# Kernel tuning notes

Hardware: AMD Instinct MI355X
Metric: run time of the kernel (lower is better)

Reference implementation:

```python
import jax, jax.numpy as jnp
import numpy as np

GAMMA = 1.0
SENTINEL = 999.0

def spike_mp(in_mat, gamma):
    # in_mat: [B, N, F]. Weighted-median-style threshold crossing (TTFS spike time).
    in_mat = jnp.sort(in_mat, axis=1)
    B, N, F = in_mat.shape
    cs = jnp.cumsum(in_mat, axis=1) + gamma
    denom = jnp.arange(1, N + 1, dtype=in_mat.dtype)[None, :, None]
    cs = cs / denom  # candidate spike times
    pad_hi = jnp.full((B, 1, F), SENTINEL, dtype=in_mat.dtype)
    pad_lo = jnp.zeros((B, 1, F), dtype=in_mat.dtype)
    arr_1 = jnp.concatenate([pad_hi, cs], axis=1)      # [B, N+1, F]
    arr_2 = jnp.concatenate([in_mat, pad_lo], axis=1)  # [B, N+1, F]
    out = jnp.where(arr_1 > arr_2, SENTINEL, arr_1)
    out = jnp.min(out, axis=1)                          # [B, F]
    out = jnp.where(out == SENTINEL, arr_1[:, -1], out)
    return out

def reference(x, W):
    # x: [B, In], W: [In, Out]. The original python concat-loop is a tile ->
    # expressed here via broadcasting to avoid materializing copies early.
    xb = x[:, :, None]                      # [B, In, 1]
    plus_in = 2.0 + xb                      # 1 + x + 1
    minus_in = 2.0 - xb                     # 1 - x + 1
    plus_w = (0.5 * (3.0 + W))[None]        # [1, In, Out]
    minus_w = (0.5 * (3.0 - W))[None]
    z_plus = jnp.concatenate([plus_in + plus_w, minus_in + minus_w], axis=1)   # [B, 2In, Out]
    z_minus = jnp.concatenate([plus_in + minus_w, minus_in + plus_w], axis=1)  # [B, 2In, Out]
    return jax.nn.relu(spike_mp(z_plus, GAMMA) - spike_mp(z_minus, GAMMA))

def setup_inputs() -> dict:
    key = jax.random.key(0)
    k1, k2 = jax.random.split(key)
    x = jax.random.uniform(k1, (32, 1024), dtype=jnp.float32)
    # GlorotNormal-ish init, clipped to [-3, 3] per the constraint
    std = np.sqrt(2.0 / (1024 + 512)).astype(np.float32)
    W = jnp.clip(jax.random.normal(k2, (1024, 512), dtype=jnp.float32) * std, -3.0, 3.0)
    return {"x": x, "W": W}
```

## Files before the change

### kernel.cpp

```cpp
#include <hip/hip_runtime.h>
#include <math.h>

#define NB 32
#define NN 1024
#define NF 512

__global__ __launch_bounds__(256) void transpose_w_k(const float* __restrict__ W,
                                                     float* __restrict__ Wt) {
    __shared__ float tile[32][33];
    int n0 = blockIdx.x * 32;
    int f0 = blockIdx.y * 32;
    int tx = threadIdx.x & 31;
    int ty = threadIdx.x >> 5;
#pragma unroll
    for (int r = 0; r < 32; r += 8) {
        tile[ty + r][tx] = W[(n0 + ty + r) * NF + (f0 + tx)];
    }
    __syncthreads();
#pragma unroll
    for (int r = 0; r < 32; r += 8) {
        Wt[(f0 + ty + r) * NN + (n0 + tx)] = tile[tx][ty + r];
    }
}

#define DPP_XOR1        0xB1
#define DPP_XOR2        0x4E
#define DPP_HALF_MIRROR 0x141
#define DPP_MIRROR      0x140
#define DPP_BCAST15     0x142
#define DPP_BCAST31     0x143

template <int CTRL>
__device__ __forceinline__ float dpp_mov(float v) {
    return __int_as_float(__builtin_amdgcn_update_dpp(
        0, __float_as_int(v), CTRL, 0xf, 0xf, true));
}

__device__ __forceinline__ float wave_sum_u(float v) {
    v += dpp_mov<DPP_XOR1>(v);
    v += dpp_mov<DPP_XOR2>(v);
    v += dpp_mov<DPP_HALF_MIRROR>(v);
    v += dpp_mov<DPP_MIRROR>(v);
    v += dpp_mov<DPP_BCAST15>(v);
    v += dpp_mov<DPP_BCAST31>(v);
    return __int_as_float(__builtin_amdgcn_readlane(__float_as_int(v), 63));
}
__device__ __forceinline__ float wave_max_u(float v) {
    v = fmaxf(v, dpp_mov<DPP_XOR1>(v));
    v = fmaxf(v, dpp_mov<DPP_XOR2>(v));
    v = fmaxf(v, dpp_mov<DPP_HALF_MIRROR>(v));
    v = fmaxf(v, dpp_mov<DPP_MIRROR>(v));
    v = fmaxf(v, dpp_mov<DPP_BCAST15>(v));
    v = fmaxf(v, dpp_mov<DPP_BCAST31>(v));
    return __int_as_float(__builtin_amdgcn_readlane(__float_as_int(v), 63));
}

__device__ __forceinline__ float fast_sqrt(float v) { return __builtin_amdgcn_sqrtf(v); }
__device__ __forceinline__ float fast_rcp(float v)  { return __builtin_amdgcn_rcpf(v); }

#define COLD_SOLVE(MARR, SV, MV, NEGV, RESV)                                     \
    if (NEGV) {                                                                  \
        float t_ = fminf(fmaxf(2.0f * (SV - fast_sqrt(SV)) * (1.0f/1024.0f), 0.0f), MV); \
        _Pragma("unroll 1")                                                      \
        for (int s_ = 0; s_ < 20; ++s_) {                                        \
            float ss_ = 0.f; int c_ = 0;                                         \
            _Pragma("unroll")                                                    \
            for (int j_ = 0; j_ < 16; ++j_) {                                    \
                bool pr_ = (MARR[j_] >= t_);                                     \
                c_ += (int)__popcll(__ballot(pr_));                              \
                ss_ += pr_ ? MARR[j_] : 0.0f;                                    \
            }                                                                    \
            ss_ = wave_sum_u(ss_);                                               \
            float fc_ = (float)c_;                                               \
            float E_ = ss_ - t_ * fc_;                                           \
            float d_ = (E_ >= 1.0f) ? 2.0f * (E_ - fast_sqrt(E_)) : (E_ - 1.0f); \
            t_ = fminf(fmaxf(t_ + d_ * fast_rcp(fc_), 0.0f), MV);                \
        }                                                                        \
        RESV = -t_;                                                              \
    } else {                                                                     \
        float u_ = (1.0f - SV) * (1.0f/1024.0f);                                 \
        _Pragma("unroll 1")                                                      \
        for (int s_ = 0; s_ < 12; ++s_) {                                        \
            float s2_ = 0.f; int c2_ = 0;                                        \
            _Pragma("unroll")                                                    \
            for (int j_ = 0; j_ < 16; ++j_) {                                    \
                bool pr_ = (MARR[j_] <= u_);                                     \
                c2_ += (int)__popcll(__ballot(pr_));                             \
                s2_ += pr_ ? MARR[j_] : 0.0f;                                    \
            }                                                                    \
            s2_ = wave_sum_u(s2_);                                               \
            u_ = (1.0f - SV + s2_) * fast_rcp(1024.0f + (float)c2_);             \
        }                                                                        \
        RESV = u_;                                                               \
    }

__global__ __launch_bounds__(256) void spike_main_k(const float* __restrict__ x,
                                                    const float* __restrict__ W,
                                                    const float* __restrict__ Wt,
                                                    int use_wt,
                                                    float* __restrict__ out) {
    int bid  = blockIdx.x;
    int b    = bid >> 7;
    int fg   = bid & 127;
    int wave = threadIdx.x >> 6;
    int lane = threadIdx.x & 63;
    int f    = fg * 4 + wave;

    float mp[16], mm[16];
    float sp0 = 0.f, sm0 = 0.f, xp0 = 0.f, xm0 = 0.f;

    if (use_wt) {
        const float4* x4 = reinterpret_cast<const float4*>(x + (size_t)b * NN);
        const float4* w4 = reinterpret_cast<const float4*>(Wt + (size_t)f * NN);
#pragma unroll
        for (int j = 0; j < 4; ++j) {
            float4 xv = x4[lane + 64 * j];
            float4 wv = w4[lane + 64 * j];
            float ap, am;
            ap = fabsf(xv.x + 0.5f * wv.x); am = fabsf(xv.x - 0.5f * wv.x);
            mp[4*j+0] = ap; mm[4*j+0] = am; sp0 += ap; sm0 += am;
            xp0 = fmaxf(xp0, ap); xm0 = fmaxf(xm0, am);
            ap = fabsf(xv.y + 0.5f * wv.y); am = fabsf(xv.y - 0.5f * wv.y);
            mp[4*j+1] = ap; mm[4*j+1] = am; sp0 += ap; sm0 += am;
            xp0 = fmaxf(xp0, ap); xm0 = fmaxf(xm0, am);
            ap = fabsf(xv.z + 0.5f * wv.z); am = fabsf(xv.z - 0.5f * wv.z);
            mp[4*j+2] = ap; mm[4*j+2] = am; sp0 += ap; sm0 += am;
            xp0 = fmaxf(xp0, ap); xm0 = fmaxf(xm0, am);
            ap = fabsf(xv.w + 0.5f * wv.w); am = fabsf(xv.w - 0.5f * wv.w);
            mp[4*j+3] = ap; mm[4*j+3] = am; sp0 += ap; sm0 += am;
            xp0 = fmaxf(xp0, ap); xm0 = fmaxf(xm0, am);
        }
    } else {
#pragma unroll
        for (int j = 0; j < 16; ++j) {
            int n = lane + 64 * j;
            float xv = x[(size_t)b * NN + n];
            float wv = W[(size_t)n * NF + f];
            float ap = fabsf(xv + 0.5f * wv);
            float am = fabsf(xv - 0.5f * wv);
            mp[j] = ap; mm[j] = am;
            sp0 += ap; sm0 += am;
            xp0 = fmaxf(xp0, ap); xm0 = fmaxf(xm0, am);
        }
    }

#pragma unroll
    for (int j = 0; j < 16; ++j) {
        asm volatile("" : "+v"(mp[j]), "+v"(mm[j]));
    }

    float Sp = wave_sum_u(sp0);
    float Sm = wave_sum_u(sm0);
    float Mp = wave_max_u(xp0);
    float Mm = wave_max_u(xm0);

    const bool neg_p = (Sp >= 1.0f);
    const bool neg_m = (Sm >= 1.0f);

    float up_out, um_out;

    if (neg_p && neg_m) {
        float tp = fminf(fmaxf(2.0f * (Sp - fast_sqrt(Sp)) * (1.0f / 1024.0f), 0.0f), Mp);
        float tm = fminf(fmaxf(2.0f * (Sm - fast_sqrt(Sm)) * (1.0f / 1024.0f), 0.0f), Mm);
#pragma unroll
        for (int s = 0; s < 5; ++s) {
            float ssp = 0.f, ssm = 0.f;
            int cp = 0, cm = 0;
#pragma unroll
            for (int j = 0; j < 16; ++j) {
                bool prp = (mp[j] >= tp);
                bool prm = (mm[j] >= tm);
                cp += (int)__popcll(__ballot(prp));
                cm += (int)__popcll(__ballot(prm));
                ssp += prp ? mp[j] : 0.0f;
                ssm += prm ? mm[j] : 0.0f;
            }
            ssp = wave_sum_u(ssp);
            ssm = wave_sum_u(ssm);
            float fcp = (float)cp, fcm = (float)cm;
            float Ep = ssp - tp * fcp;
            float Em = ssm - tm * fcm;
            float dp = (Ep >= 1.0f) ? 2.0f * (Ep - fast_sqrt(Ep)) : (Ep - 1.0f);
            float dm = (Em >= 1.0f) ? 2.0f * (Em - fast_sqrt(Em)) : (Em - 1.0f);
            tp = fminf(fmaxf(tp + dp * fast_rcp(fcp), 0.0f), Mp);
            tm = fminf(fmaxf(tm + dm * fast_rcp(fcm), 0.0f), Mm);
        }
        up_out = -tp;
        um_out = -tm;
    } else {
        COLD_SOLVE(mp, Sp, Mp, neg_p, up_out);
        COLD_SOLVE(mm, Sm, Mm, neg_m, um_out);
    }

    if (lane == 0) out[(size_t)b * NF + f] = fmaxf(up_out - um_out, 0.0f);
}

extern "C" void kernel_launch(void* const* d_in, const int* in_sizes, int n_in,
                              void* d_out, int out_size, void* d_ws, size_t ws_size,
                              hipStream_t stream) {
    const float* x = (const float*)d_in[0];
    const float* W = (const float*)d_in[1];
    float* out = (float*)d_out;

    const size_t wt_bytes = (size_t)NN * NF * sizeof(float);
    int use_wt = (ws_size >= wt_bytes) ? 1 : 0;
    float* Wt = (float*)d_ws;

    if (use_wt) {
        dim3 g(NN / 32, NF / 32);
        transpose_w_k<<<g, 256, 0, stream>>>(W, Wt);
    }
    spike_main_k<<<NB * (NF / 4), 256, 0, stream>>>(x, W, Wt, use_wt, out);
}
```

Before: 31.07 us.

## Use secant-based threshold solve and process two features per wave

```diff
diff --git a/kernel.cpp b/kernel.cpp
--- a/kernel.cpp
+++ b/kernel.cpp
@@ -57,6 +57,55 @@
 
 __device__ __forceinline__ float fast_sqrt(float v) { return __builtin_amdgcn_sqrtf(v); }
 __device__ __forceinline__ float fast_rcp(float v)  { return __builtin_amdgcn_rcpf(v); }
+
+#define FAST_SOLVE(MP, MM, SP, SM, MPX, MMX, TP_OUT, TM_OUT)                          \
+    {                                                                                 \
+        float tpp_ = 0.0f, Epp_ = SP;                                                 \
+        float tmp2_ = 0.0f, Emp_ = SM;                                                \
+        float tp_ = fminf(2.0f * (SP - fast_sqrt(SP)) * (1.0f/1024.0f), MPX);         \
+        float tm_ = fminf(2.0f * (SM - fast_sqrt(SM)) * (1.0f/1024.0f), MMX);         \
+        _Pragma("unroll")                                                             \
+        for (int s_ = 0; s_ < 5; ++s_) {                                              \
+            float ep_ = 0.f, em_ = 0.f;                                               \
+            _Pragma("unroll")                                                         \
+            for (int j_ = 0; j_ < 16; ++j_) {                                         \
+                ep_ += fmaxf(MP[j_] - tp_, 0.0f);                                     \
+                em_ += fmaxf(MM[j_] - tm_, 0.0f);                                     \
+            }                                                                         \
+            ep_ = wave_sum_u(ep_);                                                    \
+            em_ = wave_sum_u(em_);                                                    \
+            float rp_, rm_, rpp_, rmp_;                                               \
+            if (s_ < 3) { rp_ = fast_sqrt(ep_);  rm_ = fast_sqrt(em_);                \
+                          rpp_ = fast_sqrt(Epp_); rmp_ = fast_sqrt(Emp_); }           \
+            else        { rp_ = ep_; rm_ = em_; rpp_ = Epp_; rmp_ = Emp_; }           \
+            float denp_ = rp_ - rpp_, denm_ = rm_ - rmp_;                             \
+            float stp_ = (denp_ != 0.0f)                                              \
+                       ? (tp_ - tpp_) * (1.0f - rp_) * fast_rcp(denp_) : 0.0f;        \
+            float stm_ = (denm_ != 0.0f)                                              \
+                       ? (tm_ - tmp2_) * (1.0f - rm_) * fast_rcp(denm_) : 0.0f;       \
+            tpp_ = tp_; Epp_ = ep_; tmp2_ = tm_; Emp_ = em_;                          \
+            tp_ = fminf(fmaxf(tp_ + stp_, 0.0f), MPX);                                \
+            tm_ = fminf(fmaxf(tm_ + stm_, 0.0f), MMX);                                \
+        }                                                                             \
+        _Pragma("unroll")                                                             \
+        for (int q_ = 0; q_ < 2; ++q_) {                                              \
+            float ep_ = 0.f, cp_ = 0.f, em_ = 0.f, cm_ = 0.f;                         \
+            _Pragma("unroll")                                                         \
+            for (int j_ = 0; j_ < 16; ++j_) {                                         \
+                float dp_ = MP[j_] - tp_;                                             \
+                float dm_ = MM[j_] - tm_;                                             \
+                bool ap_ = (dp_ >= 0.0f);                                             \
+                bool am_ = (dm_ >= 0.0f);                                             \
+                ep_ += ap_ ? dp_ : 0.0f;  cp_ += ap_ ? 1.0f : 0.0f;                   \
+                em_ += am_ ? dm_ : 0.0f;  cm_ += am_ ? 1.0f : 0.0f;                   \
+            }                                                                         \
+            ep_ = wave_sum_u(ep_); cp_ = wave_sum_u(cp_);                             \
+            em_ = wave_sum_u(em_); cm_ = wave_sum_u(cm_);                             \
+            tp_ = fminf(fmaxf(tp_ + (ep_ - 1.0f) * fast_rcp(cp_), 0.0f), MPX);        \
+            tm_ = fminf(fmaxf(tm_ + (em_ - 1.0f) * fast_rcp(cm_), 0.0f), MMX);        \
+        }                                                                             \
+        TP_OUT = tp_; TM_OUT = tm_;                                                   \
+    }
 
 #define COLD_SOLVE(MARR, SV, MV, NEGV, RESV)                                     \
     if (NEGV) {                                                                  \
@@ -94,105 +143,96 @@
         RESV = u_;                                                               \
     }
 
+#define SETUP4(XV, WV, MP, MM, BASE, SPV, SMV, XPV, XMV)                         \
+    {                                                                            \
+        float ap_, am_;                                                          \
+        ap_ = fabsf(XV.x + 0.5f * WV.x); am_ = fabsf(XV.x - 0.5f * WV.x);        \
+        MP[BASE+0] = ap_; MM[BASE+0] = am_; SPV += ap_; SMV += am_;              \
+        XPV = fmaxf(XPV, ap_); XMV = fmaxf(XMV, am_);                            \
+        ap_ = fabsf(XV.y + 0.5f * WV.y); am_ = fabsf(XV.y - 0.5f * WV.y);        \
+        MP[BASE+1] = ap_; MM[BASE+1] = am_; SPV += ap_; SMV += am_;              \
+        XPV = fmaxf(XPV, ap_); XMV = fmaxf(XMV, am_);                            \
+        ap_ = fabsf(XV.z + 0.5f * WV.z); am_ = fabsf(XV.z - 0.5f * WV.z);        \
+        MP[BASE+2] = ap_; MM[BASE+2] = am_; SPV += ap_; SMV += am_;              \
+        XPV = fmaxf(XPV, ap_); XMV = fmaxf(XMV, am_);                            \
+        ap_ = fabsf(XV.w + 0.5f * WV.w); am_ = fabsf(XV.w - 0.5f * WV.w);        \
+        MP[BASE+3] = ap_; MM[BASE+3] = am_; SPV += ap_; SMV += am_;              \
+        XPV = fmaxf(XPV, ap_); XMV = fmaxf(XMV, am_);                            \
+    }
+
 __global__ __launch_bounds__(256) void spike_main_k(const float* __restrict__ x,
-                                                    const float* __restrict__ W,
                                                     const float* __restrict__ Wt,
-                                                    int use_wt,
                                                     float* __restrict__ out) {
     int bid  = blockIdx.x;
-    int b    = bid >> 7;
-    int fg   = bid & 127;
+    int b    = bid >> 6;
+    int fg   = bid & 63;
     int wave = threadIdx.x >> 6;
     int lane = threadIdx.x & 63;
-    int f    = fg * 4 + wave;
-
-    float mp[16], mm[16];
-    float sp0 = 0.f, sm0 = 0.f, xp0 = 0.f, xm0 = 0.f;
-
-    if (use_wt) {
-        const float4* x4 = reinterpret_cast<const float4*>(x + (size_t)b * NN);
-        const float4* w4 = reinterpret_cast<const float4*>(Wt + (size_t)f * NN);
-#pragma unroll
-        for (int j = 0; j < 4; ++j) {
-            float4 xv = x4[lane + 64 * j];
-            float4 wv = w4[lane + 64 * j];
-            float ap, am;
-            ap = fabsf(xv.x + 0.5f * wv.x); am = fabsf(xv.x - 0.5f * wv.x);
-            mp[4*j+0] = ap; mm[4*j+0] = am; sp0 += ap; sm0 += am;
-            xp0 = fmaxf(xp0, ap); xm0 = fmaxf(xm0, am);
-            ap = fabsf(xv.y + 0.5f * wv.y); am = fabsf(xv.y - 0.5f * wv.y);
-            mp[4*j+1] = ap; mm[4*j+1] = am; sp0 += ap; sm0 += am;
-            xp0 = fmaxf(xp0, ap); xm0 = fmaxf(xm0, am);
-            ap = fabsf(xv.z + 0.5f * wv.z); am = fabsf(xv.z - 0.5f * wv.z);
-            mp[4*j+2] = ap; mm[4*j+2] = am; sp0 += ap; sm0 += am;
-            xp0 = fmaxf(xp0, ap); xm0 = fmaxf(xm0, am);
-            ap = fabsf(xv.w + 0.5f * wv.w); am = fabsf(xv.w - 0.5f * wv.w);
-            mp[4*j+3] = ap; mm[4*j+3] = am; sp0 += ap; sm0 += am;
-            xp0 = fmaxf(xp0, ap); xm0 = fmaxf(xm0, am);
-        }
-    } else {
-#pragma unroll
-        for (int j = 0; j < 16; ++j) {
-            int n = lane + 64 * j;
-            float xv = x[(size_t)b * NN + n];
-            float wv = W[(size_t)n * NF + f];
-            float ap = fabsf(xv + 0.5f * wv);
-            float am = fabsf(xv - 0.5f * wv);
-            mp[j] = ap; mm[j] = am;
-            sp0 += ap; sm0 += am;
-            xp0 = fmaxf(xp0, ap); xm0 = fmaxf(xm0, am);
-        }
-    }
+    int f1   = fg * 4 + wave;
+    int f2   = f1 + 256;
+
+    const float4* x4  = reinterpret_cast<const float4*>(x + (size_t)b * NN);
+    const float4* wa4 = reinterpret_cast<const float4*>(Wt + (size_t)f1 * NN);
+    const float4* wb4 = reinterpret_cast<const float4*>(Wt + (size_t)f2 * NN);
+
+    float4 xr0 = x4[lane +   0], xr1 = x4[lane +  64],
+           xr2 = x4[lane + 128], xr3 = x4[lane + 192];
+    float4 wa0 = wa4[lane +   0], wa1 = wa4[lane +  64],
+           wa2 = wa4[lane + 128], wa3 = wa4[lane + 192];
+    float4 wb0 = wb4[lane +   0], wb1 = wb4[lane +  64],
+           wb2 = wb4[lane + 128], wb3 = wb4[lane + 192];
+
+    float mp1[16], mm1[16], mp2[16], mm2[16];
+    float sp1 = 0.f, sm1 = 0.f, xp1 = 0.f, xm1 = 0.f;
+    float sp2 = 0.f, sm2 = 0.f, xp2 = 0.f, xm2 = 0.f;
+
+    SETUP4(xr0, wa0, mp1, mm1,  0, sp1, sm1, xp1, xm1);
+    SETUP4(xr1, wa1, mp1, mm1,  4, sp1, sm1, xp1, xm1);
+    SETUP4(xr2, wa2, mp1, mm1,  8, sp1, sm1, xp1, xm1);
+    SETUP4(xr3, wa3, mp1, mm1, 12, sp1, sm1, xp1, xm1);
+    SETUP4(xr0, wb0, mp2, mm2,  0, sp2, sm2, xp2, xm2);
+    SETUP4(xr1, wb1, mp2, mm2,  4, sp2, sm2, xp2, xm2);
+    SETUP4(xr2, wb2, mp2, mm2,  8, sp2, sm2, xp2, xm2);
+    SETUP4(xr3, wb3, mp2, mm2, 12, sp2, sm2, xp2, xm2);
 
 #pragma unroll
     for (int j = 0; j < 16; ++j) {
-        asm volatile("" : "+v"(mp[j]), "+v"(mm[j]));
-    }
-
-    float Sp = wave_sum_u(sp0);
-    float Sm = wave_sum_u(sm0);
-    float Mp = wave_max_u(xp0);
-    float Mm = wave_max_u(xm0);
-
-    const bool neg_p = (Sp >= 1.0f);
-    const bool neg_m = (Sm >= 1.0f);
-
-    float up_out, um_out;
-
-    if (neg_p && neg_m) {
-        float tp = fminf(fmaxf(2.0f * (Sp - fast_sqrt(Sp)) * (1.0f / 1024.0f), 0.0f), Mp);
-        float tm = fminf(fmaxf(2.0f * (Sm - fast_sqrt(Sm)) * (1.0f / 1024.0f), 0.0f), Mm);
-#pragma unroll
-        for (int s = 0; s < 5; ++s) {
-            float ssp = 0.f, ssm = 0.f;
-            int cp = 0, cm = 0;
-#pragma unroll
-            for (int j = 0; j < 16; ++j) {
-                bool prp = (mp[j] >= tp);
-                bool prm = (mm[j] >= tm);
-                cp += (int)__popcll(__ballot(prp));
-                cm += (int)__popcll(__ballot(prm));
-                ssp += prp ? mp[j] : 0.0f;
-                ssm += prm ? mm[j] : 0.0f;
-            }
-            ssp = wave_sum_u(ssp);
-            ssm = wave_sum_u(ssm);
-            float fcp = (float)cp, fcm = (float)cm;
-            float Ep = ssp - tp * fcp;
-            float Em = ssm - tm * fcm;
-            float dp = (Ep >= 1.0f) ? 2.0f * (Ep - fast_sqrt(Ep)) : (Ep - 1.0f);
-            float dm = (Em >= 1.0f) ? 2.0f * (Em - fast_sqrt(Em)) : (Em - 1.0f);
-            tp = fminf(fmaxf(tp + dp * fast_rcp(fcp), 0.0f), Mp);
-            tm = fminf(fmaxf(tm + dm * fast_rcp(fcm), 0.0f), Mm);
-        }
-        up_out = -tp;
-        um_out = -tm;
+        asm volatile("" : "+v"(mp1[j]), "+v"(mm1[j]), "+v"(mp2[j]), "+v"(mm2[j]));
+    }
+
+    float Sp1 = wave_sum_u(sp1), Sm1 = wave_sum_u(sm1);
+    float Mp1 = wave_max_u(xp1), Mm1 = wave_max_u(xm1);
+    float Sp2 = wave_sum_u(sp2), Sm2 = wave_sum_u(sm2);
+    float Mp2 = wave_max_u(xp2), Mm2 = wave_max_u(xm2);
+
+    float o1, o2;
+
+    if (Sp1 >= 1.0f && Sm1 >= 1.0f) {
+        float tp1, tm1;
+        FAST_SOLVE(mp1, mm1, Sp1, Sm1, Mp1, Mm1, tp1, tm1);
+        o1 = fmaxf(tm1 - tp1, 0.0f);
     } else {
-        COLD_SOLVE(mp, Sp, Mp, neg_p, up_out);
-        COLD_SOLVE(mm, Sm, Mm, neg_m, um_out);
-    }
-
-    if (lane == 0) out[(size_t)b * NF + f] = fmaxf(up_out - um_out, 0.0f);
+        float up1, um1;
+        COLD_SOLVE(mp1, Sp1, Mp1, (Sp1 >= 1.0f), up1);
+        COLD_SOLVE(mm1, Sm1, Mm1, (Sm1 >= 1.0f), um1);
+        o1 = fmaxf(up1 - um1, 0.0f);
+    }
+
+    if (Sp2 >= 1.0f && Sm2 >= 1.0f) {
+        float tp2, tm2;
+        FAST_SOLVE(mp2, mm2, Sp2, Sm2, Mp2, Mm2, tp2, tm2);
+        o2 = fmaxf(tm2 - tp2, 0.0f);
+    } else {
+        float up2, um2;
+        COLD_SOLVE(mp2, Sp2, Mp2, (Sp2 >= 1.0f), up2);
+        COLD_SOLVE(mm2, Sm2, Mm2, (Sm2 >= 1.0f), um2);
+        o2 = fmaxf(up2 - um2, 0.0f);
+    }
+
+    if (lane == 0) {
+        out[(size_t)b * NF + f1] = o1;
+        out[(size_t)b * NF + f2] = o2;
+    }
 }
 
 extern "C" void kernel_launch(void* const* d_in, const int* in_sizes, int n_in,
@@ -201,14 +241,9 @@
     const float* x = (const float*)d_in[0];
     const float* W = (const float*)d_in[1];
     float* out = (float*)d_out;
-
-    const size_t wt_bytes = (size_t)NN * NF * sizeof(float);
-    int use_wt = (ws_size >= wt_bytes) ? 1 : 0;
     float* Wt = (float*)d_ws;
 
-    if (use_wt) {
-        dim3 g(NN / 32, NF / 32);
-        transpose_w_k<<<g, 256, 0, stream>>>(W, Wt);
-    }
-    spike_main_k<<<NB * (NF / 4), 256, 0, stream>>>(x, W, Wt, use_wt, out);
-}
+    dim3 g(NN / 32, NF / 32);
+    transpose_w_k<<<g, 256, 0, stream>>>(W, Wt);
+    spike_main_k<<<NB * (NF / 8), 256, 0, stream>>>(x, Wt, out);
+}
```

New measurement: 39.47 us. 27.1% more time.

## Split plus and minus solves across separate waves and combine via shared memory

Applied to the files above, without the earlier changes.

```diff
diff --git a/kernel.cpp b/kernel.cpp
--- a/kernel.cpp
+++ b/kernel.cpp
@@ -58,11 +58,12 @@
 __device__ __forceinline__ float fast_sqrt(float v) { return __builtin_amdgcn_sqrtf(v); }
 __device__ __forceinline__ float fast_rcp(float v)  { return __builtin_amdgcn_rcpf(v); }
 
-#define COLD_SOLVE(MARR, SV, MV, NEGV, RESV)                                     \
-    if (NEGV) {                                                                  \
-        float t_ = fminf(fmaxf(2.0f * (SV - fast_sqrt(SV)) * (1.0f/1024.0f), 0.0f), MV); \
-        _Pragma("unroll 1")                                                      \
-        for (int s_ = 0; s_ < 20; ++s_) {                                        \
+#define HYBRID5(MARR, SV, MV, RES_T)                                             \
+    {                                                                            \
+        float t_ = fminf(fmaxf(2.0f * (SV - fast_sqrt(SV)) * (1.0f/1024.0f),     \
+                               0.0f), MV);                                       \
+        _Pragma("unroll")                                                        \
+        for (int s_ = 0; s_ < 5; ++s_) {                                         \
             float ss_ = 0.f; int c_ = 0;                                         \
             _Pragma("unroll")                                                    \
             for (int j_ = 0; j_ < 16; ++j_) {                                    \
@@ -76,8 +77,11 @@
             float d_ = (E_ >= 1.0f) ? 2.0f * (E_ - fast_sqrt(E_)) : (E_ - 1.0f); \
             t_ = fminf(fmaxf(t_ + d_ * fast_rcp(fc_), 0.0f), MV);                \
         }                                                                        \
-        RESV = -t_;                                                              \
-    } else {                                                                     \
+        RES_T = t_;                                                              \
+    }
+
+#define COLD_POS(MARR, SV, RES_U)                                                \
+    {                                                                            \
         float u_ = (1.0f - SV) * (1.0f/1024.0f);                                 \
         _Pragma("unroll 1")                                                      \
         for (int s_ = 0; s_ < 12; ++s_) {                                        \
@@ -91,108 +95,64 @@
             s2_ = wave_sum_u(s2_);                                               \
             u_ = (1.0f - SV + s2_) * fast_rcp(1024.0f + (float)c2_);             \
         }                                                                        \
-        RESV = u_;                                                               \
+        RES_U = u_;                                                              \
     }
 
-__global__ __launch_bounds__(256) void spike_main_k(const float* __restrict__ x,
-                                                    const float* __restrict__ W,
-                                                    const float* __restrict__ Wt,
-                                                    int use_wt,
-                                                    float* __restrict__ out) {
+__global__ __launch_bounds__(512, 8) void spike_main_k(const float* __restrict__ x,
+                                                       const float* __restrict__ Wt,
+                                                       float* __restrict__ out) {
+    __shared__ float ures[8];
+
     int bid  = blockIdx.x;
     int b    = bid >> 7;
     int fg   = bid & 127;
     int wave = threadIdx.x >> 6;
     int lane = threadIdx.x & 63;
-    int f    = fg * 4 + wave;
+    int side = wave >> 2;
+    int fi   = wave & 3;
+    int f    = fg * 4 + fi;
 
-    float mp[16], mm[16];
-    float sp0 = 0.f, sm0 = 0.f, xp0 = 0.f, xm0 = 0.f;
+    const float4* x4 = reinterpret_cast<const float4*>(x + (size_t)b * NN);
+    const float4* w4 = reinterpret_cast<const float4*>(Wt + (size_t)f * NN);
 
-    if (use_wt) {
-        const float4* x4 = reinterpret_cast<const float4*>(x + (size_t)b * NN);
-        const float4* w4 = reinterpret_cast<const float4*>(Wt + (size_t)f * NN);
+    const float h = side ? -0.5f : 0.5f;
+
+    float m[16];
+    float s0 = 0.f, x0 = 0.f;
 #pragma unroll
-        for (int j = 0; j < 4; ++j) {
-            float4 xv = x4[lane + 64 * j];
-            float4 wv = w4[lane + 64 * j];
-            float ap, am;
-            ap = fabsf(xv.x + 0.5f * wv.x); am = fabsf(xv.x - 0.5f * wv.x);
-            mp[4*j+0] = ap; mm[4*j+0] = am; sp0 += ap; sm0 += am;
-            xp0 = fmaxf(xp0, ap); xm0 = fmaxf(xm0, am);
-            ap = fabsf(xv.y + 0.5f * wv.y); am = fabsf(xv.y - 0.5f * wv.y);
-            mp[4*j+1] = ap; mm[4*j+1] = am; sp0 += ap; sm0 += am;
-            xp0 = fmaxf(xp0, ap); xm0 = fmaxf(xm0, am);
-            ap = fabsf(xv.z + 0.5f * wv.z); am = fabsf(xv.z - 0.5f * wv.z);
-            mp[4*j+2] = ap; mm[4*j+2] = am; sp0 += ap; sm0 += am;
-            xp0 = fmaxf(xp0, ap); xm0 = fmaxf(xm0, am);
-            ap = fabsf(xv.w + 0.5f * wv.w); am = fabsf(xv.w - 0.5f * wv.w);
-            mp[4*j+3] = ap; mm[4*j+3] = am; sp0 += ap; sm0 += am;
-            xp0 = fmaxf(xp0, ap); xm0 = fmaxf(xm0, am);
-        }
-    } else {
-#pragma unroll
-        for (int j = 0; j < 16; ++j) {
-            int n = lane + 64 * j;
-            float xv = x[(size_t)b * NN + n];
-            float wv = W[(size_t)n * NF + f];
-            float ap = fabsf(xv + 0.5f * wv);
-            float am = fabsf(xv - 0.5f * wv);
-            mp[j] = ap; mm[j] = am;
-            sp0 += ap; sm0 += am;
-            xp0 = fmaxf(xp0, ap); xm0 = fmaxf(xm0, am);
-        }
+    for (int j = 0; j < 4; ++j) {
+        float4 xv = x4[lane + 64 * j];
+        float4 wv = w4[lane + 64 * j];
+        float a;
+        a = fabsf(fmaf(h, wv.x, xv.x)); m[4*j+0] = a; s0 += a; x0 = fmaxf(x0, a);
+        a = fabsf(fmaf(h, wv.y, xv.y)); m[4*j+1] = a; s0 += a; x0 = fmaxf(x0, a);
+        a = fabsf(fmaf(h, wv.z, xv.z)); m[4*j+2] = a; s0 += a; x0 = fmaxf(x0, a);
+        a = fabsf(fmaf(h, wv.w, xv.w)); m[4*j+3] = a; s0 += a; x0 = fmaxf(x0, a);
     }
 
 #pragma unroll
     for (int j = 0; j < 16; ++j) {
-        asm volatile("" : "+v"(mp[j]), "+v"(mm[j]));
+        asm volatile("" : "+v"(m[j]));
     }
 
-    float Sp = wave_sum_u(sp0);
-    float Sm = wave_sum_u(sm0);
-    float Mp = wave_max_u(xp0);
-    float Mm = wave_max_u(xm0);
+    float S = wave_sum_u(s0);
+    float M = wave_max_u(x0);
 
-    const bool neg_p = (Sp >= 1.0f);
-    const bool neg_m = (Sm >= 1.0f);
-
-    float up_out, um_out;
-
-    if (neg_p && neg_m) {
-        float tp = fminf(fmaxf(2.0f * (Sp - fast_sqrt(Sp)) * (1.0f / 1024.0f), 0.0f), Mp);
-        float tm = fminf(fmaxf(2.0f * (Sm - fast_sqrt(Sm)) * (1.0f / 1024.0f), 0.0f), Mm);
-#pragma unroll
-        for (int s = 0; s < 5; ++s) {
-            float ssp = 0.f, ssm = 0.f;
-            int cp = 0, cm = 0;
-#pragma unroll
-            for (int j = 0; j < 16; ++j) {
-                bool prp = (mp[j] >= tp);
-                bool prm = (mm[j] >= tm);
-                cp += (int)__popcll(__ballot(prp));
-                cm += (int)__popcll(__ballot(prm));
-                ssp += prp ? mp[j] : 0.0f;
-                ssm += prm ? mm[j] : 0.0f;
-            }
-            ssp = wave_sum_u(ssp);
-            ssm = wave_sum_u(ssm);
-            float fcp = (float)cp, fcm = (float)cm;
-            float Ep = ssp - tp * fcp;
-            float Em = ssm - tm * fcm;
-            float dp = (Ep >= 1.0f) ? 2.0f * (Ep - fast_sqrt(Ep)) : (Ep - 1.0f);
-            float dm = (Em >= 1.0f) ? 2.0f * (Em - fast_sqrt(Em)) : (Em - 1.0f);
-            tp = fminf(fmaxf(tp + dp * fast_rcp(fcp), 0.0f), Mp);
-            tm = fminf(fmaxf(tm + dm * fast_rcp(fcm), 0.0f), Mm);
-        }
-        up_out = -tp;
-        um_out = -tm;
+    float u;
+    if (S >= 1.0f) {
+        float t;
+        HYBRID5(m, S, M, t);
+        u = -t;
     } else {
-        COLD_SOLVE(mp, Sp, Mp, neg_p, up_out);
-        COLD_SOLVE(mm, Sm, Mm, neg_m, um_out);
+        COLD_POS(m, S, u);
     }
 
-    if (lane == 0) out[(size_t)b * NF + f] = fmaxf(up_out - um_out, 0.0f);
+    if (lane == 0) ures[wave] = u;
+    __syncthreads();
+
+    if (wave < 4 && lane == 0) {
+        out[(size_t)b * NF + f] = fmaxf(ures[wave] - ures[wave + 4], 0.0f);
+    }
 }
 
 extern "C" void kernel_launch(void* const* d_in, const int* in_sizes, int n_in,
@@ -201,14 +161,9 @@
     const float* x = (const float*)d_in[0];
     const float* W = (const float*)d_in[1];
     float* out = (float*)d_out;
-
-    const size_t wt_bytes = (size_t)NN * NF * sizeof(float);
-    int use_wt = (ws_size >= wt_bytes) ? 1 : 0;
     float* Wt = (float*)d_ws;
 
-    if (use_wt) {
-        dim3 g(NN / 32, NF / 32);
-        transpose_w_k<<<g, 256, 0, stream>>>(W, Wt);
-    }
-    spike_main_k<<<NB * (NF / 4), 256, 0, stream>>>(x, W, Wt, use_wt, out);
+    dim3 g(NN / 32, NF / 32);
+    transpose_w_k<<<g, 256, 0, stream>>>(W, Wt);
+    spike_main_k<<<4096, 512, 0, stream>>>(x, Wt, out);
 }
```

Measured after the change: 28.85 us, median of 2. 1.08x faster.
